# Performance work log

Measured on AMD Instinct MI355X. Metric: run time of the kernel, lower is better.

The kernel has to match this reference:

```python
import jax, jax.numpy as jnp
import numpy as np

B, F, T_IN, T_OUT = 64, 256, 4096, 4096
BN_EPS = 1e-5


def setup_inputs() -> dict:
    key = jax.random.key(0)
    k1, k2, k3 = jax.random.split(key, 3)
    data = jax.random.normal(k1, (B, F, T_IN), dtype=jnp.float32)
    # matches init_params(): translate ~ N(0, 0.1^2), scale ~ N(0, 0.15^2)
    translate = jax.random.normal(k2, (F,), dtype=jnp.float32) * 0.1
    scale = jax.random.normal(k3, (F,), dtype=jnp.float32) * 0.15
    gamma = jnp.ones((F,), dtype=jnp.float32)
    beta = jnp.zeros((F,), dtype=jnp.float32)
    return {"data": data, "translate": translate, "scale": scale,
            "gamma": gamma, "beta": beta}


def _affine_resample(data, translate, scale):
    # Per-feature 1D affine resample, equivalent to torch affine_grid +
    # bilinear grid_sample with align_corners=False, padding_mode='zeros'.
    # theta = [[s, 0, s*t], [0, 1, 0]] per feature; H=1 so the y-axis is
    # degenerate (y' = 0 -> full weight on row 0).
    Bv, Fv, Tin = data.shape
    s = jnp.exp(scale / 5.0)                                  # [F]
    x = (2.0 * jnp.arange(T_OUT, dtype=jnp.float32) + 1.0) / T_OUT - 1.0  # [T_out]
    coord = s[:, None] * x[None, :] + (s * translate)[:, None]           # [F, T_out]
    ix = ((coord + 1.0) * Tin - 1.0) / 2.0                    # unnormalize
    i0 = jnp.floor(ix)
    w = ix - i0                                               # bilinear weight
    i0i = i0.astype(jnp.int32)
    i1i = i0i + 1
    valid0 = (i0i >= 0) & (i0i < Tin)
    valid1 = (i1i >= 0) & (i1i < Tin)
    i0c = jnp.clip(i0i, 0, Tin - 1)
    i1c = jnp.clip(i1i, 0, Tin - 1)
    # gather per (feature, out-pos), broadcast across batch: [B, F, T_out]
    v0 = jnp.take_along_axis(data, jnp.broadcast_to(i0c[None], (Bv, Fv, T_OUT)), axis=2)
    v1 = jnp.take_along_axis(data, jnp.broadcast_to(i1c[None], (Bv, Fv, T_OUT)), axis=2)
    v0 = jnp.where(valid0[None], v0, 0.0)
    v1 = jnp.where(valid1[None], v1, 0.0)
    return v0 * (1.0 - w)[None] + v1 * w[None]


def _batchnorm1d(x, gamma, beta):
    # BatchNorm1d in training mode: biased stats over (batch, time)
    mean = jnp.mean(x, axis=(0, 2), keepdims=True)
    var = jnp.mean(jnp.square(x - mean), axis=(0, 2), keepdims=True)
    xhat = (x - mean) * jax.lax.rsqrt(var + BN_EPS)
    return xhat * gamma[None, :, None] + beta[None, :, None]


def reference(data, translate, scale, gamma, beta):
    filtered = _affine_resample(data, translate, scale)   # [B, F, T_out]
    return _batchnorm1d(filtered, gamma, beta)
```

## Files before the change

### kernel.cpp

```cpp
#include <hip/hip_runtime.h>

#define NB 64
#define NF 256
#define TIN 4096
#define TOUT 4096
#define BN_EPS 1e-5f

typedef float f32x4 __attribute__((ext_vector_type(4)));

__device__ __forceinline__ void waveReduce2(float& s, float& q) {
    #pragma unroll
    for (int off = 32; off > 0; off >>= 1) {
        s += __shfl_down(s, off, 64);
        q += __shfl_down(q, off, 64);
    }
}

__device__ __forceinline__ f32x4 resample4(const float* __restrict__ row,
                                           int t0, float s, float C) {
    f32x4 r;
    const float tf = (float)t0;
    #pragma unroll
    for (int j = 0; j < 4; ++j) {
        float ix = fmaf(s, tf + (float)j, C);
        float i0f = floorf(ix);
        float w = ix - i0f;
        int i0 = (int)i0f;
        int i1 = i0 + 1;
        float v0 = (i0 >= 0 && i0 < TIN) ? row[i0] : 0.0f;
        float v1 = (i1 >= 0 && i1 < TIN) ? row[i1] : 0.0f;
        r[j] = fmaf(w, v1 - v0, v0);
    }
    return r;
}

__device__ __forceinline__ void stage_row(const float* __restrict__ row_g,
                                          float* __restrict__ row) {
    const f32x4* src4 = (const f32x4*)row_g;
    f32x4* dst4 = (f32x4*)row;
    #pragma unroll
    for (int i = 0; i < TIN / 4 / 256; ++i)
        dst4[threadIdx.x + i * 256] = src4[threadIdx.x + i * 256];
}

__device__ __forceinline__ float2 row_consts(const float* translate,
                                             const float* scale, int f) {
    float s = expf(scale[f] / 5.0f);
    float st = s * translate[f];
    float C = (s * (1.0f / (float)TOUT - 1.0f) + st + 1.0f) * (0.5f * (float)TIN)
              - 0.5f;
    return make_float2(s, C);
}

__global__ __launch_bounds__(256) void k_resample_stats(
    const float* __restrict__ data,
    const float* __restrict__ translate,
    const float* __restrict__ scale,
    float2* __restrict__ partials)
{
    const int blk = blockIdx.x;
    const int f = blk & (NF - 1);
    const int b = blk >> 8;
    const float* row_g = data + ((size_t)b * NF + f) * (size_t)TIN;

    __shared__ float row[TIN];
    __shared__ float2 wred[4];

    stage_row(row_g, row);
    __syncthreads();

    const float2 sc = row_consts(translate, scale, f);

    float sum = 0.0f, sq = 0.0f;
    #pragma unroll
    for (int k = 0; k < 4; ++k) {
        int t0 = (threadIdx.x + k * 256) * 4;
        f32x4 v = resample4(row, t0, sc.x, sc.y);
        sum += v.x + v.y + v.z + v.w;
        sq += v.x * v.x + v.y * v.y + v.z * v.z + v.w * v.w;
    }

    waveReduce2(sum, sq);
    const int lane = threadIdx.x & 63;
    const int wid = threadIdx.x >> 6;
    if (lane == 0) wred[wid] = make_float2(sum, sq);
    __syncthreads();
    if (threadIdx.x == 0) {
        float S = 0.0f, Q = 0.0f;
        #pragma unroll
        for (int i = 0; i < 4; ++i) { S += wred[i].x; Q += wred[i].y; }
        partials[blk] = make_float2(S, Q);
    }
}

__global__ __launch_bounds__(256) void k_apply(
    const float* __restrict__ data,
    const float* __restrict__ translate,
    const float* __restrict__ scale,
    const float2* __restrict__ partials,
    const float* __restrict__ gamma,
    const float* __restrict__ beta,
    float* __restrict__ out)
{
    const int blk = blockIdx.x;
    const int f = blk & (NF - 1);
    const int b = blk >> 8;
    const size_t rowbase = ((size_t)b * NF + f) * (size_t)TIN;
    const float* row_g = data + rowbase;
    float* out_row = out + rowbase;

    __shared__ float row[TIN];
    __shared__ float2 s_ac;

    stage_row(row_g, row);

    if (threadIdx.x < 64) {
        float2 p = partials[(size_t)threadIdx.x * NF + f];
        float S = p.x, Q = p.y;
        waveReduce2(S, Q);
        if (threadIdx.x == 0) {
            const float invN = 1.0f / (float)(NB * TOUT);
            float mean = S * invN;
            float var = Q * invN - mean * mean;
            float inv = 1.0f / sqrtf(var + BN_EPS);
            float a = gamma[f] * inv;
            s_ac = make_float2(a, beta[f] - mean * a);
        }
    }
    __syncthreads();

    const float2 sc = row_consts(translate, scale, f);
    const float a = s_ac.x;
    const float c = s_ac.y;

    #pragma unroll
    for (int k = 0; k < 4; ++k) {
        int t0 = (threadIdx.x + k * 256) * 4;
        f32x4 v = resample4(row, t0, sc.x, sc.y);
        v.x = v.x * a + c;
        v.y = v.y * a + c;
        v.z = v.z * a + c;
        v.w = v.w * a + c;
        __builtin_nontemporal_store(v, (f32x4*)(out_row + t0));
    }
}

extern "C" void kernel_launch(void* const* d_in, const int* in_sizes, int n_in,
                              void* d_out, int out_size, void* d_ws, size_t ws_size,
                              hipStream_t stream) {
    const float* data      = (const float*)d_in[0];
    const float* translate = (const float*)d_in[1];
    const float* scale     = (const float*)d_in[2];
    const float* gamma     = (const float*)d_in[3];
    const float* beta      = (const float*)d_in[4];
    float* out = (float*)d_out;

    float2* partials = (float2*)d_ws;

    k_resample_stats<<<NB * NF, 256, 0, stream>>>(data, translate, scale, partials);
    k_apply<<<NB * NF, 256, 0, stream>>>(data, translate, scale, partials,
                                         gamma, beta, out);
}
```

Before: 128.6 us.

## Store resampled values as fp16 intermediate instead of recomputing in apply pass

The stats kernel now writes the resampled values to a half-precision workspace buffer. The apply kernel reads that buffer instead of restaging the input row and redoing the gather-based resample. This removes the second LDS staging and interpolation work but adds an extra write and read of an intermediate, so total memory traffic stays about the same. It also loses precision by rounding values to fp16 before normalization, and the input read is switched to a nontemporal load.

```diff
diff --git a/kernel.cpp b/kernel.cpp
--- a/kernel.cpp
+++ b/kernel.cpp
@@ -7,6 +7,8 @@
 #define BN_EPS 1e-5f
 
 typedef float f32x4 __attribute__((ext_vector_type(4)));
+typedef _Float16 f16x4 __attribute__((ext_vector_type(4)));
+typedef _Float16 f16x8 __attribute__((ext_vector_type(8)));
 
 __device__ __forceinline__ void waveReduce2(float& s, float& q) {
     #pragma unroll
@@ -34,15 +36,6 @@
     return r;
 }
 
-__device__ __forceinline__ void stage_row(const float* __restrict__ row_g,
-                                          float* __restrict__ row) {
-    const f32x4* src4 = (const f32x4*)row_g;
-    f32x4* dst4 = (f32x4*)row;
-    #pragma unroll
-    for (int i = 0; i < TIN / 4 / 256; ++i)
-        dst4[threadIdx.x + i * 256] = src4[threadIdx.x + i * 256];
-}
-
 __device__ __forceinline__ float2 row_consts(const float* translate,
                                              const float* scale, int f) {
     float s = expf(scale[f] / 5.0f);
@@ -56,17 +49,27 @@
     const float* __restrict__ data,
     const float* __restrict__ translate,
     const float* __restrict__ scale,
-    float2* __restrict__ partials)
+    float2* __restrict__ partials,
+    _Float16* __restrict__ mid)
 {
     const int blk = blockIdx.x;
     const int f = blk & (NF - 1);
     const int b = blk >> 8;
-    const float* row_g = data + ((size_t)b * NF + f) * (size_t)TIN;
+    const size_t rowbase = ((size_t)b * NF + f) * (size_t)TIN;
+    const float* row_g = data + rowbase;
+    _Float16* mid_row = mid + rowbase;
 
     __shared__ float row[TIN];
     __shared__ float2 wred[4];
 
-    stage_row(row_g, row);
+    {
+        const f32x4* src4 = (const f32x4*)row_g;
+        f32x4* dst4 = (f32x4*)row;
+        #pragma unroll
+        for (int i = 0; i < TIN / 4 / 256; ++i)
+            dst4[threadIdx.x + i * 256] =
+                __builtin_nontemporal_load(&src4[threadIdx.x + i * 256]);
+    }
     __syncthreads();
 
     const float2 sc = row_consts(translate, scale, f);
@@ -78,6 +81,8 @@
         f32x4 v = resample4(row, t0, sc.x, sc.y);
         sum += v.x + v.y + v.z + v.w;
         sq += v.x * v.x + v.y * v.y + v.z * v.z + v.w * v.w;
+        f16x4 h = __builtin_convertvector(v, f16x4);
+        *(f16x4*)(mid_row + t0) = h;
     }
 
     waveReduce2(sum, sq);
@@ -94,9 +99,7 @@
 }
 
 __global__ __launch_bounds__(256) void k_apply(
-    const float* __restrict__ data,
-    const float* __restrict__ translate,
-    const float* __restrict__ scale,
+    const _Float16* __restrict__ mid,
     const float2* __restrict__ partials,
     const float* __restrict__ gamma,
     const float* __restrict__ beta,
@@ -106,13 +109,10 @@
     const int f = blk & (NF - 1);
     const int b = blk >> 8;
     const size_t rowbase = ((size_t)b * NF + f) * (size_t)TIN;
-    const float* row_g = data + rowbase;
+    const _Float16* mid_row = mid + rowbase;
     float* out_row = out + rowbase;
 
-    __shared__ float row[TIN];
     __shared__ float2 s_ac;
-
-    stage_row(row_g, row);
 
     if (threadIdx.x < 64) {
         float2 p = partials[(size_t)threadIdx.x * NF + f];
@@ -129,19 +129,22 @@
     }
     __syncthreads();
 
-    const float2 sc = row_consts(translate, scale, f);
     const float a = s_ac.x;
     const float c = s_ac.y;
 
     #pragma unroll
-    for (int k = 0; k < 4; ++k) {
-        int t0 = (threadIdx.x + k * 256) * 4;
-        f32x4 v = resample4(row, t0, sc.x, sc.y);
-        v.x = v.x * a + c;
-        v.y = v.y * a + c;
-        v.z = v.z * a + c;
-        v.w = v.w * a + c;
-        __builtin_nontemporal_store(v, (f32x4*)(out_row + t0));
+    for (int k = 0; k < 2; ++k) {
+        int t0 = (threadIdx.x + k * 256) * 8;
+        f16x8 h = *(const f16x8*)(mid_row + t0);
+        f32x4 lo, hi;
+        #pragma unroll
+        for (int j = 0; j < 4; ++j) { lo[j] = (float)h[j]; hi[j] = (float)h[j+4]; }
+        lo.x = lo.x * a + c; lo.y = lo.y * a + c;
+        lo.z = lo.z * a + c; lo.w = lo.w * a + c;
+        hi.x = hi.x * a + c; hi.y = hi.y * a + c;
+        hi.z = hi.z * a + c; hi.w = hi.w * a + c;
+        __builtin_nontemporal_store(lo, (f32x4*)(out_row + t0));
+        __builtin_nontemporal_store(hi, (f32x4*)(out_row + t0 + 4));
     }
 }
 
@@ -156,8 +159,9 @@
     float* out = (float*)d_out;
 
     float2* partials = (float2*)d_ws;
+    _Float16* mid = (_Float16*)((char*)d_ws + (1 << 20));
 
-    k_resample_stats<<<NB * NF, 256, 0, stream>>>(data, translate, scale, partials);
-    k_apply<<<NB * NF, 256, 0, stream>>>(data, translate, scale, partials,
-                                         gamma, beta, out);
+    k_resample_stats<<<NB * NF, 256, 0, stream>>>(data, translate, scale,
+                                                  partials, mid);
+    k_apply<<<NB * NF, 256, 0, stream>>>(mid, partials, gamma, beta, out);
 }
```

Measured after the change: 166.4 us. 29.3% more time.
